# Optimization experiments

Hardware: AMD Instinct MI355X
Metric: run time of the kernel (lower is better)

The kernel has to match this reference:

```python
import jax, jax.numpy as jnp
import numpy as np

NUM_HEADS = 32
NUM_KV_HEADS = 8
HEAD_DIM = 64


def rotate_half(x):
    x1, x2 = jnp.split(x, 2, axis=-1)
    return jnp.concatenate((-x2, x1), axis=-1)


def setup_inputs() -> dict:
    key = jax.random.key(0)
    ks = jax.random.split(key, 7)
    B, S, H = 2, 2048, 2048
    hidden_states = jax.random.normal(ks[0], (B, S, H), dtype=jnp.float32)
    # RoPE angles: build realistic cos/sin from inv_freq for positions 0..S-1
    inv_freq = 1.0 / (10000.0 ** (np.arange(0, HEAD_DIM, 2, dtype=np.float32) / HEAD_DIM))
    t = np.arange(S, dtype=np.float32)
    freqs = np.outer(t, inv_freq)  # [S, HEAD_DIM/2]
    emb = np.concatenate([freqs, freqs], axis=-1)  # [S, HEAD_DIM]
    cos = jnp.broadcast_to(jnp.cos(emb)[None], (B, S, HEAD_DIM)).astype(jnp.float32)
    sin = jnp.broadcast_to(jnp.sin(emb)[None], (B, S, HEAD_DIM)).astype(jnp.float32)
    scale = 1.0 / np.sqrt(H)
    Wq = jax.random.normal(ks[1], (NUM_HEADS * HEAD_DIM, H), dtype=jnp.float32) * scale
    Wk = jax.random.normal(ks[2], (NUM_KV_HEADS * HEAD_DIM, H), dtype=jnp.float32) * scale
    Wv = jax.random.normal(ks[3], (NUM_KV_HEADS * HEAD_DIM, H), dtype=jnp.float32) * scale
    Wo = jax.random.normal(ks[4], (H, H), dtype=jnp.float32) * scale
    return {"hidden_states": hidden_states, "cos": cos, "sin": sin,
            "Wq": Wq, "Wk": Wk, "Wv": Wv, "Wo": Wo}


def reference(hidden_states, cos, sin, Wq, Wk, Wv, Wo):
    B, S, H = hidden_states.shape
    hd = HEAD_DIM
    # QKV projections (torch Linear: y = x @ W.T)
    q = jnp.einsum('bsi,oi->bso', hidden_states, Wq).reshape(B, S, NUM_HEADS, hd).transpose(0, 2, 1, 3)
    k = jnp.einsum('bsi,oi->bso', hidden_states, Wk).reshape(B, S, NUM_KV_HEADS, hd).transpose(0, 2, 1, 3)
    v = jnp.einsum('bsi,oi->bso', hidden_states, Wv).reshape(B, S, NUM_KV_HEADS, hd).transpose(0, 2, 1, 3)
    # RoPE: cos/sin [B,S,hd] -> [B,1,S,hd] broadcast over heads
    c = cos[:, None, :, :]
    s = sin[:, None, :, :]
    q = q * c + rotate_half(q) * s
    k = k * c + rotate_half(k) * s
    # GQA: repeat kv heads to match query heads
    groups = NUM_HEADS // NUM_KV_HEADS
    k = jnp.repeat(k, groups, axis=1)
    v = jnp.repeat(v, groups, axis=1)
    scaling = hd ** -0.5
    scores = jnp.einsum('bhqd,bhkd->bhqk', q, k) * scaling
    causal = jnp.tril(jnp.ones((S, S), dtype=bool))
    scores = jnp.where(causal, scores, jnp.finfo(scores.dtype).min)
    attn = jax.nn.softmax(scores, axis=-1)
    y = jnp.einsum('bhqk,bhkd->bhqd', attn, v)
    y = y.transpose(0, 2, 1, 3).reshape(B, S, H)
    return jnp.einsum('bsi,oi->bso', y, Wo)
```

## Files before the change

kernel.cpp:

```cpp
#include <hip/hip_runtime.h>

typedef __bf16 bf16_t;
typedef bf16_t bf16x8 __attribute__((ext_vector_type(8)));
typedef bf16_t bf16x4 __attribute__((ext_vector_type(4)));
typedef float f32x4 __attribute__((ext_vector_type(4)));
typedef float f32x16 __attribute__((ext_vector_type(16)));

#define MFMA16(a, b, c) __builtin_amdgcn_mfma_f32_16x16x32_bf16(a, b, c, 0, 0, 0)
#define MFMA32(a, b, c) __builtin_amdgcn_mfma_f32_32x32x16_bf16(a, b, c, 0, 0, 0)

#define GLOAD16(gsrc, ldst)                                            \
  __builtin_amdgcn_global_load_lds(                                    \
      (const __attribute__((address_space(1))) void*)(gsrc),           \
      (__attribute__((address_space(3))) void*)(ldst), 16, 0, 0)

constexpr int B_ = 2, S_ = 2048, H_ = 2048, NH = 32, NKV = 8, HD = 64;
constexpr int NQKV = NH * HD + 2 * NKV * HD;
constexpr int M_ROWS = B_ * S_;
constexpr float QSCALE = 0.125f * 1.4426950408889634f;

__global__ __launch_bounds__(256) void cvt_kernel(const float* __restrict__ in,
                                                  bf16_t* __restrict__ out, int n8) {
  int i = blockIdx.x * 256 + threadIdx.x;
  if (i >= n8) return;
  const float4* p = (const float4*)(in + (size_t)i * 8);
  float4 a = p[0], b = p[1];
  bf16x8 o;
  o[0] = (bf16_t)a.x; o[1] = (bf16_t)a.y; o[2] = (bf16_t)a.z; o[3] = (bf16_t)a.w;
  o[4] = (bf16_t)b.x; o[5] = (bf16_t)b.y; o[6] = (bf16_t)b.z; o[7] = (bf16_t)b.w;
  *(bf16x8*)(out + (size_t)i * 8) = o;
}

__global__ __launch_bounds__(256) void cvt3_kernel(const float* __restrict__ s0,
                                                   const float* __restrict__ s1,
                                                   const float* __restrict__ s2,
                                                   bf16_t* __restrict__ out) {
  int i = blockIdx.x * 256 + threadIdx.x;
  const float* src;
  long off;
  if (i < 524288) { src = s0; off = i; }
  else if (i < 655360) { src = s1; off = i - 524288; }
  else { src = s2; off = i - 655360; }
  const float4* p = (const float4*)(src + off * 8);
  float4 a = p[0], b = p[1];
  bf16x8 o;
  o[0] = (bf16_t)a.x; o[1] = (bf16_t)a.y; o[2] = (bf16_t)a.z; o[3] = (bf16_t)a.w;
  o[4] = (bf16_t)b.x; o[5] = (bf16_t)b.y; o[6] = (bf16_t)b.z; o[7] = (bf16_t)b.w;
  *(bf16x8*)(out + (size_t)i * 8) = o;
}

template <int MODE>
__global__ __launch_bounds__(256) void gemm_bt(const bf16_t* __restrict__ A,
                                               const bf16_t* __restrict__ Bm,
                                               float* __restrict__ Cf,
                                               bf16_t* __restrict__ Cb,
                                               bf16_t* __restrict__ vTo,
                                               const float* __restrict__ cosb,
                                               const float* __restrict__ sinb,
                                               int M, int N, int K) {
  __shared__ __align__(16) bf16_t As[2][128 * 32];
  __shared__ __align__(16) bf16_t Bs[2][128 * 32];
  const int t = threadIdx.x;
  const int lane = t & 63, w = t >> 6;
  const int l15 = lane & 15, l4 = lane >> 4;
  const int wm = w >> 1, wn = w & 1;
  const long Ar0 = (long)blockIdx.y * 128;
  const long Br0 = (long)blockIdx.x * 128;
  const int nt = K >> 5;

  const int scol = ((lane & 3) ^ ((lane >> 3) & 3)) * 8;
  const int srow = lane >> 2;
  auto stage = [&](int kt, int buf) {
#pragma unroll
    for (int c = 0; c < 2; ++c) {
      const int i = w * 2 + c;
      const bf16_t* gA = A + (Ar0 + i * 16 + srow) * (long)K + kt * 32 + scol;
      const bf16_t* gB = Bm + (Br0 + i * 16 + srow) * (long)K + kt * 32 + scol;
      GLOAD16(gA, &As[buf][i * 512]);
      GLOAD16(gB, &Bs[buf][i * 512]);
    }
  };

  f32x4 acc[4][4] = {};
  stage(0, 0);
  __syncthreads();
  int cur = 0;
  const int rsw = l4 ^ ((l15 >> 1) & 3);
  for (int kt = 0; kt < nt; ++kt) {
    if (kt + 1 < nt) stage(kt + 1, cur ^ 1);
    bf16x8 af[4], bfr[4];
#pragma unroll
    for (int mf = 0; mf < 4; ++mf)
      af[mf] = *(const bf16x8*)&As[cur][(wm * 64 + mf * 16 + l15) * 32 + rsw * 8];
#pragma unroll
    for (int nf = 0; nf < 4; ++nf)
      bfr[nf] = *(const bf16x8*)&Bs[cur][(wn * 64 + nf * 16 + l15) * 32 + rsw * 8];
#pragma unroll
    for (int mf = 0; mf < 4; ++mf)
#pragma unroll
      for (int nf = 0; nf < 4; ++nf)
        acc[mf][nf] = MFMA16(af[mf], bfr[nf], acc[mf][nf]);
    __syncthreads();
    cur ^= 1;
  }

  if (MODE == 0) {
#pragma unroll
    for (int mf = 0; mf < 4; ++mf)
#pragma unroll
      for (int nf = 0; nf < 4; ++nf)
#pragma unroll
        for (int r = 0; r < 4; ++r) {
          long row = Ar0 + wm * 64 + mf * 16 + l4 * 4 + r;
          long col = Br0 + wn * 64 + nf * 16 + l15;
          Cf[row * N + col] = acc[mf][nf][r];
        }
  } else {
    const long col0 = Br0 + wn * 64;
    if (col0 < 2560) {
      const float scl = (col0 < 2048) ? QSCALE : 1.0f;
#pragma unroll
      for (int mf = 0; mf < 4; ++mf) {
        const long row = Ar0 + wm * 64 + mf * 16 + l4 * 4;
#pragma unroll
        for (int nf = 0; nf < 2; ++nf) {
          const int d = nf * 16 + l15;
#pragma unroll
          for (int r = 0; r < 4; ++r) {
            const float c = cosb[(row + r) * 64 + d] * scl;
            const float s = sinb[(row + r) * 64 + d] * scl;
            const float x1 = acc[mf][nf][r], x2 = acc[mf][nf + 2][r];
            Cb[(row + r) * N + col0 + d]      = (bf16_t)(x1 * c - x2 * s);
            Cb[(row + r) * N + col0 + d + 32] = (bf16_t)(x2 * c + x1 * s);
          }
        }
      }
    } else {
#pragma unroll
      for (int mf = 0; mf < 4; ++mf) {
        const long row = Ar0 + wm * 64 + mf * 16 + l4 * 4;
        const int bb = (int)(row >> 11);
        const int ss = (int)(row & 2047);
#pragma unroll
        for (int nf = 0; nf < 4; ++nf) {
          const int vd = (int)(col0 - 2560) + nf * 16 + l15;
          bf16x4 o;
#pragma unroll
          for (int r = 0; r < 4; ++r) o[r] = (bf16_t)acc[mf][nf][r];
          *(bf16x4*)&vTo[((long)bb * 512 + vd) * 2048 + ss] = o;
        }
      }
    }
  }
}

__device__ __forceinline__ unsigned pkbf16(float lo, float hi) {
  union { bf16_t h[2]; unsigned u; } x;
  x.h[0] = (bf16_t)lo;
  x.h[1] = (bf16_t)hi;
  return x.u;
}

__global__ __launch_bounds__(128) void attn32_kernel(const bf16_t* __restrict__ qkv,
                                                     const bf16_t* __restrict__ vT,
                                                     bf16_t* __restrict__ y) {
  const int h = blockIdx.y;
  const int b = blockIdx.z;
  const int kvh = h >> 2;
  const int t = threadIdx.x, lane = t & 63, w = t >> 6;
  const int l31 = lane & 31, hd = lane >> 5;
  const long bS = (long)b * S_;

  __shared__ __align__(16) bf16_t Klds[2][64 * 64];
  __shared__ __align__(16) bf16_t Vlds[2][64 * 64];

  const bf16_t* kbase = qkv + bS * NQKV + NH * HD + kvh * 64;
  const bf16_t* vbase = vT + ((long)(b * NKV + kvh)) * 64 * S_;

  const int row0 = t >> 3;
  const int slot = t & 7;
  const int wslot8 = ((slot ^ (row0 & 7)) << 3);
  bf16x8 kreg[4], vreg[4];

  auto ldG = [&](int kv0) {
#pragma unroll
    for (int c = 0; c < 4; ++c) {
      kreg[c] = *(const bf16x8*)(kbase + (long)(kv0 + row0 + 16 * c) * NQKV + slot * 8);
      vreg[c] = *(const bf16x8*)(vbase + (long)(row0 + 16 * c) * S_ + kv0 + slot * 8);
    }
  };
  auto wrLDS = [&](int buf) {
#pragma unroll
    for (int c = 0; c < 4; ++c) {
      *(bf16x8*)&Klds[buf][(row0 + 16 * c) * 64 + wslot8] = kreg[c];
      *(bf16x8*)&Vlds[buf][(row0 + 16 * c) * 64 + wslot8] = vreg[c];
    }
  };

  for (int half = 0; half < 2; ++half) {
    const int qt = half ? (int)blockIdx.x : 31 - (int)blockIdx.x;
    const int q0w = qt * 64 + w * 32;
    const int myq = q0w + l31;
    const int NT = qt + 1;

    const bf16_t* qp = qkv + (bS + myq) * NQKV + h * 64 + hd * 8;
    bf16x8 qf[4];
#pragma unroll
    for (int ks = 0; ks < 4; ++ks) qf[ks] = *(const bf16x8*)(qp + ks * 16);

    f32x16 yac[2] = {};
    float m = -1e30f, l = 0.f;

    ldG(0);
    wrLDS(0);
    __syncthreads();

    for (int kt = 0; kt < NT; ++kt) {
      const int buf = kt & 1;
      const int kv0 = kt * 64;
      if (kt + 1 < NT) ldG(kv0 + 64);

      f32x16 sac[2] = {};
      __builtin_amdgcn_s_setprio(1);
#pragma unroll
      for (int ks = 0; ks < 4; ++ks)
#pragma unroll
        for (int kb = 0; kb < 2; ++kb) {
          const int row = kb * 32 + l31;
          const bf16x8 kf =
              *(const bf16x8*)&Klds[buf][row * 64 + (((2 * ks + hd) ^ (row & 7)) << 3)];
          sac[kb] = MFMA32(kf, qf[ks], sac[kb]);
        }
      __builtin_amdgcn_s_setprio(0);
      if (kv0 + 63 > q0w) {
#pragma unroll
        for (int kb = 0; kb < 2; ++kb)
#pragma unroll
          for (int r = 0; r < 16; ++r) {
            const int kv = kv0 + kb * 32 + (r & 3) + 8 * (r >> 2) + 4 * hd;
            if (kv > myq) sac[kb][r] = -3.0e38f;
          }
      }
      float pm4[8], sm4[8];
#pragma unroll
      for (int g = 0; g < 8; ++g) {
        const int kb = g >> 2, r = (g & 3) * 4;
        pm4[g] = fmaxf(fmaxf(sac[kb][r], sac[kb][r + 1]),
                       fmaxf(sac[kb][r + 2], sac[kb][r + 3]));
      }
      float pm = fmaxf(fmaxf(fmaxf(pm4[0], pm4[1]), fmaxf(pm4[2], pm4[3])),
                       fmaxf(fmaxf(pm4[4], pm4[5]), fmaxf(pm4[6], pm4[7])));
      pm = fmaxf(pm, __shfl_xor(pm, 32, 64));
      if (!__all(pm <= m + 8.f)) {
        const float mnew = fmaxf(m, pm);
        const float sc = __builtin_amdgcn_exp2f(m - mnew);
        l *= sc;
        yac[0] *= sc;
        yac[1] *= sc;
        m = mnew;
      }
#pragma unroll
      for (int kb = 0; kb < 2; ++kb)
#pragma unroll
        for (int r = 0; r < 16; ++r)
          sac[kb][r] = __builtin_amdgcn_exp2f(sac[kb][r] - m);
#pragma unroll
      for (int g = 0; g < 8; ++g) {
        const int kb = g >> 2, r = (g & 3) * 4;
        sm4[g] = (sac[kb][r] + sac[kb][r + 1]) + (sac[kb][r + 2] + sac[kb][r + 3]);
      }
      l += ((sm4[0] + sm4[1]) + (sm4[2] + sm4[3])) +
           ((sm4[4] + sm4[5]) + (sm4[6] + sm4[7]));
#pragma unroll
      for (int ks = 0; ks < 4; ++ks) {
        const int kb = ks >> 1;
        const int Bv = 8 * (ks & 1);
        unsigned a0 = pkbf16(sac[kb][Bv + 0], sac[kb][Bv + 1]);
        unsigned b0 = pkbf16(sac[kb][Bv + 4], sac[kb][Bv + 5]);
        unsigned a1 = pkbf16(sac[kb][Bv + 2], sac[kb][Bv + 3]);
        unsigned b1 = pkbf16(sac[kb][Bv + 6], sac[kb][Bv + 7]);
        asm("v_permlane32_swap_b32 %0, %1" : "+v"(a0), "+v"(b0));
        asm("v_permlane32_swap_b32 %0, %1" : "+v"(a1), "+v"(b1));
        union { unsigned u[4]; bf16x8 v; } pu;
        pu.u[0] = a0; pu.u[1] = a1; pu.u[2] = b0; pu.u[3] = b1;
        __builtin_amdgcn_s_setprio(1);
#pragma unroll
        for (int db = 0; db < 2; ++db) {
          const int row = db * 32 + l31;
          const bf16x8 vf =
              *(const bf16x8*)&Vlds[buf][row * 64 + (((2 * ks + hd) ^ (row & 7)) << 3)];
          yac[db] = MFMA32(vf, pu.v, yac[db]);
        }
        __builtin_amdgcn_s_setprio(0);
      }

      if (kt + 1 < NT) wrLDS(buf ^ 1);
      __syncthreads();
    }

    l += __shfl_xor(l, 32, 64);
    const float inv = __builtin_amdgcn_rcpf(l);
    bf16_t* yp = y + (bS + myq) * (long)H_ + h * 64;
#pragma unroll
    for (int db = 0; db < 2; ++db)
#pragma unroll
      for (int g = 0; g < 4; ++g) {
        bf16x4 o;
        o[0] = (bf16_t)(yac[db][4 * g + 0] * inv);
        o[1] = (bf16_t)(yac[db][4 * g + 1] * inv);
        o[2] = (bf16_t)(yac[db][4 * g + 2] * inv);
        o[3] = (bf16_t)(yac[db][4 * g + 3] * inv);
        *(bf16x4*)(yp + db * 32 + 8 * g + 4 * hd) = o;
      }
  }
}

extern "C" void kernel_launch(void* const* d_in, const int* in_sizes, int n_in,
                              void* d_out, int out_size, void* d_ws, size_t ws_size,
                              hipStream_t stream) {
  const float* hs = (const float*)d_in[0];
  const float* cosb = (const float*)d_in[1];
  const float* sinb = (const float*)d_in[2];
  const float* Wq = (const float*)d_in[3];
  const float* Wk = (const float*)d_in[4];
  const float* Wv = (const float*)d_in[5];
  const float* Wo = (const float*)d_in[6];
  float* out = (float*)d_out;

  char* ws = (char*)d_ws;
  bf16_t* hsb  = (bf16_t*)(ws);
  bf16_t* wqkv = (bf16_t*)(ws + 16777216);
  bf16_t* wo   = (bf16_t*)(ws + 29360128);
  bf16_t* qkv  = (bf16_t*)(ws + 37748736);
  bf16_t* vT   = (bf16_t*)(ws + 62914560);
  bf16_t* yb   = (bf16_t*)(ws + 67108864);

  cvt_kernel<<<4096, 256, 0, stream>>>(hs, hsb, 1048576);
  cvt3_kernel<<<3072, 256, 0, stream>>>(Wq, Wk, Wv, wqkv);
  cvt_kernel<<<2048, 256, 0, stream>>>(Wo, wo, 524288);

  gemm_bt<1><<<dim3(24, 32), 256, 0, stream>>>(hsb, wqkv, nullptr, qkv, vT,
                                               cosb, sinb, M_ROWS, NQKV, H_);
  attn32_kernel<<<dim3(16, 32, 2), 128, 0, stream>>>(qkv, vT, yb);
  gemm_bt<0><<<dim3(16, 32), 256, 0, stream>>>(yb, wo, out, nullptr, nullptr,
                                               nullptr, nullptr, M_ROWS, H_, H_);
}
```

Measured before the change: 236.7 us.

## Split RoPE and V transpose out of QKV GEMM epilogue into separate kernels

Moves the RoPE rotation and the V transposition out of the QKV GEMM epilogue into two standalone kernels. RoPE now runs with vectorized bf16x8 loads, and V is transposed through an XOR-swizzled LDS tile, replacing the scattered scalar and strided 4-element stores in the GEMM epilogue. The likely aim is a simpler, lighter GEMM epilogue with coalesced transposed writes. In exchange the pipeline gains two kernel launches and an extra read and write pass over the QKV buffer. RoPE is now applied to values already rounded to bf16, which adds a second rounding step.

```diff
diff --git a/kernel.cpp b/kernel.cpp
--- a/kernel.cpp
+++ b/kernel.cpp
@@ -49,14 +49,11 @@
   *(bf16x8*)(out + (size_t)i * 8) = o;
 }
 
-template <int MODE>
+template <bool OUT_BF16>
 __global__ __launch_bounds__(256) void gemm_bt(const bf16_t* __restrict__ A,
                                                const bf16_t* __restrict__ Bm,
                                                float* __restrict__ Cf,
                                                bf16_t* __restrict__ Cb,
-                                               bf16_t* __restrict__ vTo,
-                                               const float* __restrict__ cosb,
-                                               const float* __restrict__ sinb,
                                                int M, int N, int K) {
   __shared__ __align__(16) bf16_t As[2][128 * 32];
   __shared__ __align__(16) bf16_t Bs[2][128 * 32];
@@ -103,55 +100,72 @@
     __syncthreads();
     cur ^= 1;
   }
-
-  if (MODE == 0) {
-#pragma unroll
-    for (int mf = 0; mf < 4; ++mf)
-#pragma unroll
-      for (int nf = 0; nf < 4; ++nf)
-#pragma unroll
-        for (int r = 0; r < 4; ++r) {
-          long row = Ar0 + wm * 64 + mf * 16 + l4 * 4 + r;
-          long col = Br0 + wn * 64 + nf * 16 + l15;
-          Cf[row * N + col] = acc[mf][nf][r];
-        }
-  } else {
-    const long col0 = Br0 + wn * 64;
-    if (col0 < 2560) {
-      const float scl = (col0 < 2048) ? QSCALE : 1.0f;
-#pragma unroll
-      for (int mf = 0; mf < 4; ++mf) {
-        const long row = Ar0 + wm * 64 + mf * 16 + l4 * 4;
-#pragma unroll
-        for (int nf = 0; nf < 2; ++nf) {
-          const int d = nf * 16 + l15;
-#pragma unroll
-          for (int r = 0; r < 4; ++r) {
-            const float c = cosb[(row + r) * 64 + d] * scl;
-            const float s = sinb[(row + r) * 64 + d] * scl;
-            const float x1 = acc[mf][nf][r], x2 = acc[mf][nf + 2][r];
-            Cb[(row + r) * N + col0 + d]      = (bf16_t)(x1 * c - x2 * s);
-            Cb[(row + r) * N + col0 + d + 32] = (bf16_t)(x2 * c + x1 * s);
-          }
-        }
-      }
-    } else {
-#pragma unroll
-      for (int mf = 0; mf < 4; ++mf) {
-        const long row = Ar0 + wm * 64 + mf * 16 + l4 * 4;
-        const int bb = (int)(row >> 11);
-        const int ss = (int)(row & 2047);
-#pragma unroll
-        for (int nf = 0; nf < 4; ++nf) {
-          const int vd = (int)(col0 - 2560) + nf * 16 + l15;
-          bf16x4 o;
-#pragma unroll
-          for (int r = 0; r < 4; ++r) o[r] = (bf16_t)acc[mf][nf][r];
-          *(bf16x4*)&vTo[((long)bb * 512 + vd) * 2048 + ss] = o;
-        }
-      }
-    }
+#pragma unroll
+  for (int mf = 0; mf < 4; ++mf)
+#pragma unroll
+    for (int nf = 0; nf < 4; ++nf)
+#pragma unroll
+      for (int r = 0; r < 4; ++r) {
+        long row = Ar0 + wm * 64 + mf * 16 + l4 * 4 + r;
+        long col = Br0 + wn * 64 + nf * 16 + l15;
+        float v = acc[mf][nf][r];
+        if (OUT_BF16)
+          Cb[row * N + col] = (bf16_t)v;
+        else
+          Cf[row * N + col] = v;
+      }
+}
+
+__global__ __launch_bounds__(256) void rope_kernel(bf16_t* __restrict__ qkv,
+                                                   const float* __restrict__ cosb,
+                                                   const float* __restrict__ sinb) {
+  const int head = blockIdx.y;
+  const int i = blockIdx.x * 256 + threadIdx.x;
+  const long bs = i >> 2;
+  const int d0 = (i & 3) * 8;
+  const long base = bs * NQKV + (head < 32 ? head * 64 : 2048 + (head - 32) * 64) + d0;
+  const float scl = head < 32 ? QSCALE : 1.0f;
+  bf16x8 x1 = *(bf16x8*)(qkv + base);
+  bf16x8 x2 = *(bf16x8*)(qkv + base + 32);
+  const float4* cp = (const float4*)(cosb + bs * 64 + d0);
+  const float4* sp = (const float4*)(sinb + bs * 64 + d0);
+  const float4 c0 = cp[0], c1 = cp[1];
+  const float4 s0 = sp[0], s1 = sp[1];
+  const float cc[8] = {c0.x, c0.y, c0.z, c0.w, c1.x, c1.y, c1.z, c1.w};
+  const float ss[8] = {s0.x, s0.y, s0.z, s0.w, s1.x, s1.y, s1.z, s1.w};
+  bf16x8 y1, y2;
+#pragma unroll
+  for (int e = 0; e < 8; ++e) {
+    const float f1 = (float)x1[e], f2 = (float)x2[e];
+    y1[e] = (bf16_t)((f1 * cc[e] - f2 * ss[e]) * scl);
+    y2[e] = (bf16_t)((f2 * cc[e] + f1 * ss[e]) * scl);
   }
+  *(bf16x8*)(qkv + base) = y1;
+  *(bf16x8*)(qkv + base + 32) = y2;
+}
+
+__global__ __launch_bounds__(256) void v_transpose(const bf16_t* __restrict__ qkv,
+                                                   bf16_t* __restrict__ vT) {
+  __shared__ __align__(16) bf16_t lds[64 * 64];
+  const int b = blockIdx.z, kvh = blockIdx.y, s0 = blockIdx.x * 64;
+  const int t = threadIdx.x;
+  auto key = [](int s) { return (((s & 7) ^ ((s >> 3) & 7)) << 3); };
+  const int si = t >> 3, j8 = (t & 7) * 8;
+  const bf16_t* src = qkv + ((long)(b * S_ + s0 + si)) * NQKV + 2560 + kvh * 64 + j8;
+  *(bf16x8*)&lds[si * 64 + (j8 ^ key(si))] = *(const bf16x8*)src;
+  *(bf16x8*)&lds[(si + 32) * 64 + (j8 ^ key(si + 32))] =
+      *(const bf16x8*)(src + 32L * NQKV);
+  __syncthreads();
+  const int d = t >> 2, sg = (t & 3) * 16;
+  bf16x8 o0, o1;
+#pragma unroll
+  for (int e = 0; e < 8; ++e) {
+    o0[e] = lds[(sg + e) * 64 + (d ^ key(sg + e))];
+    o1[e] = lds[(sg + 8 + e) * 64 + (d ^ key(sg + 8 + e))];
+  }
+  bf16_t* dst = vT + ((long)(b * NKV + kvh) * 64 + d) * S_ + s0 + sg;
+  *(bf16x8*)dst = o0;
+  *(bf16x8*)(dst + 8) = o1;
 }
 
 __device__ __forceinline__ unsigned pkbf16(float lo, float hi) {
@@ -339,9 +353,11 @@
   cvt3_kernel<<<3072, 256, 0, stream>>>(Wq, Wk, Wv, wqkv);
   cvt_kernel<<<2048, 256, 0, stream>>>(Wo, wo, 524288);
 
-  gemm_bt<1><<<dim3(24, 32), 256, 0, stream>>>(hsb, wqkv, nullptr, qkv, vT,
-                                               cosb, sinb, M_ROWS, NQKV, H_);
+  gemm_bt<true><<<dim3(24, 32), 256, 0, stream>>>(hsb, wqkv, nullptr, qkv,
+                                                  M_ROWS, NQKV, H_);
+  rope_kernel<<<dim3(64, 40), 256, 0, stream>>>(qkv, cosb, sinb);
+  v_transpose<<<dim3(32, 8, 2), 256, 0, stream>>>(qkv, vT);
   attn32_kernel<<<dim3(16, 32, 2), 128, 0, stream>>>(qkv, vT, yb);
-  gemm_bt<0><<<dim3(16, 32), 256, 0, stream>>>(yb, wo, out, nullptr, nullptr,
-                                               nullptr, nullptr, M_ROWS, H_, H_);
-}
+  gemm_bt<false><<<dim3(16, 32), 256, 0, stream>>>(yb, wo, out, nullptr,
+                                                   M_ROWS, H_, H_);
+}
```

New measurement: 221.6 us. 6.4% less time.
